# Kernel optimization log

Hardware: AMD Instinct MI355X
Metric: run time of the kernel (lower is better)

The kernel has to match this reference:

```python
import jax, jax.numpy as jnp
import numpy as np
from jax import lax

GRID_W, GRID_H = 4, 4
N_NODES = GRID_W * GRID_H  # 16
N_NEIGH = 8
N_CLS = 10
BN_EPS = 1e-5


def _neighbors(i, w, h, mode=8):
    # exact port of Brain.neighbors (ordering matters for the concat)
    size = w * h
    out = []
    if i - w >= 0:
        out.append(i - w)
    if i % w != 0:
        out.append(i - 1)
    if (i + 1) % w != 0:
        out.append(i + 1)
    if i + w < size:
        out.append(i + w)
    if mode == 8:
        if i - w - 1 >= 0 and i % w != 0:
            out.append(i - w - 1)
        if i - w + 1 >= 0 and (i + 1) % w != 0:
            out.append(i - w + 1)
        if i + w - 1 < size and i % w != 0:
            out.append(i + w - 1)
        if i + w + 1 < size and (i + 1) % w != 0:
            out.append(i + w + 1)
    return out


def _neighbor_table():
    idx = np.full((N_NODES, N_NEIGH), 0, dtype=np.int32)
    mask = np.zeros((N_NODES, N_NEIGH), dtype=np.float32)
    for i in range(N_NODES):
        n = _neighbors(i, GRID_W, GRID_H, 8)
        idx[i, :len(n)] = np.array(n, dtype=np.int32)
        mask[i, :len(n)] = 1.0
    return jnp.asarray(idx), jnp.asarray(mask)


def _conv(x, w, b):
    y = lax.conv_general_dilated(x, w, (1, 1), 'SAME',
                                 dimension_numbers=('NCHW', 'OIHW', 'NCHW'))
    return y + b[None, :, None, None]


def _bn_train(x, g, b):
    # BatchNorm2d in training mode (module default): batch statistics
    mean = jnp.mean(x, axis=(0, 2, 3), keepdims=True)
    var = jnp.var(x, axis=(0, 2, 3), keepdims=True)
    xn = (x - mean) * lax.rsqrt(var + BN_EPS)
    return xn * g[None, :, None, None] + b[None, :, None, None]


def _maxpool(x):
    # MaxPool2d(kernel=3, stride=2, padding=1)
    return lax.reduce_window(x, -jnp.inf, lax.max,
                             (1, 1, 3, 3), (1, 1, 2, 2),
                             ((0, 0), (0, 0), (1, 1), (1, 1)))


def setup_inputs() -> dict:
    key = jax.random.key(0)
    ks = jax.random.split(key, 24)
    B = 128
    f32 = jnp.float32

    def rn(k, shape, scale):
        return jax.random.normal(k, shape, dtype=f32) * scale

    inp = {
        'x': rn(ks[0], (B, 3, 64, 64), 1.0),
        'cw1': rn(ks[1], (64, 3, 3, 3), 0.1), 'cb1': jnp.zeros((64,), f32),
        'bn1_g': jnp.ones((64,), f32), 'bn1_b': jnp.zeros((64,), f32),
        'cw2': rn(ks[2], (128, 64, 3, 3), 0.05), 'cb2': jnp.zeros((128,), f32),
        'bn2_g': jnp.ones((128,), f32), 'bn2_b': jnp.zeros((128,), f32),
        'cw3': rn(ks[3], (256, 128, 3, 3), 0.03), 'cb3': jnp.zeros((256,), f32),
        'cw4': rn(ks[4], (256, 256, 3, 3), 0.02), 'cb4': jnp.zeros((256,), f32),
        'cw5': rn(ks[5], (512, 256, 3, 3), 0.02), 'cb5': jnp.zeros((512,), f32),
        'cw6': rn(ks[6], (512, 512, 3, 3), 0.015), 'cb6': jnp.zeros((512,), f32),
        'cw7': rn(ks[7], (512, 512, 3, 3), 0.015), 'cb7': jnp.zeros((512,), f32),
        'W1': rn(ks[8], (N_NODES, 592, 600), 0.04), 'b1': jnp.zeros((N_NODES, 600), f32),
        'W2': rn(ks[9], (N_NODES, 600, N_CLS), 0.04), 'b2': jnp.zeros((N_NODES, N_CLS), f32),
    }
    return inp


def _backbone(x, cw1, cb1, bn1_g, bn1_b, cw2, cb2, bn2_g, bn2_b,
              cw3, cb3, cw4, cb4, cw5, cb5, cw6, cb6, cw7, cb7):
    h = _maxpool(jax.nn.relu(_bn_train(_conv(x, cw1, cb1), bn1_g, bn1_b)))
    h = _maxpool(jax.nn.relu(_bn_train(_conv(h, cw2, cb2), bn2_g, bn2_b)))
    h = jax.nn.relu(_conv(h, cw3, cb3))
    h = _maxpool(jax.nn.relu(_conv(h, cw4, cb4)))
    h = jax.nn.relu(_conv(h, cw5, cb5))
    h = _maxpool(jax.nn.relu(_conv(h, cw6, cb6)))
    h = jax.nn.relu(_conv(h, cw7, cb7))
    return h  # [B, 512, 4, 4]


def _colons(X, W1, b1, W2, b2):
    # X: [16, B, 592] -> softmax probs [16, B, 10]; per-node MLP
    h = jnp.tanh(jnp.einsum('nbi,nio->nbo', X, W1) + b1[:, None, :])
    logits = jnp.einsum('nbh,nho->nbo', h, W2) + b2[:, None, :]
    return jax.nn.softmax(logits, axis=-1)


def reference(x, cw1, cb1, bn1_g, bn1_b, cw2, cb2, bn2_g, bn2_b,
              cw3, cb3, cw4, cb4, cw5, cb5, cw6, cb6, cw7, cb7,
              W1, b1, W2, b2):
    B = x.shape[0]
    conv = _backbone(x, cw1, cb1, bn1_g, bn1_b, cw2, cb2, bn2_g, bn2_b,
                     cw3, cb3, cw4, cb4, cw5, cb5, cw6, cb6, cw7, cb7)
    conv = conv.reshape(B, 512, N_NODES)           # torch.flatten(conv, 2)
    feats = jnp.transpose(conv, (2, 0, 1))         # [16, B, 512]

    # first pass: neighbor slots are all-zero p1..p8
    zeros80 = jnp.zeros((N_NODES, B, N_NEIGH * N_CLS), dtype=x.dtype)
    preds1 = _colons(jnp.concatenate([zeros80, feats], axis=-1), W1, b1, W2, b2)

    # second pass: gather neighbor predictions (zero-padded to 8 slots)
    idx, mask = _neighbor_table()                  # [16,8] int, [16,8] float
    gathered = preds1[idx]                         # [16, 8, B, 10]
    gathered = gathered * mask[:, :, None, None]
    neigh = jnp.transpose(gathered, (0, 2, 1, 3)).reshape(N_NODES, B, N_NEIGH * N_CLS)
    preds2 = _colons(jnp.concatenate([neigh, feats], axis=-1), W1, b1, W2, b2)  # [16, B, 10]

    sum_preds = jnp.mean(preds2, axis=0)           # [B, 10]
    squared_sum_preds = sum_preds * sum_preds
    return squared_sum_preds, preds2
```

## Files before the change

### kernel.cpp

```cpp
#include <hip/hip_runtime.h>
#include <math.h>


#define BN_EPS 1e-5f

typedef _Float16 f16x8 __attribute__((ext_vector_type(8)));
typedef _Float16 f16x4 __attribute__((ext_vector_type(4)));
typedef float    f32x4v __attribute__((ext_vector_type(4)));

constexpr int ilog2c(int x) { return x <= 1 ? 0 : 1 + ilog2c(x >> 1); }

__global__ __launch_bounds__(256)
void wsplit_kernel(const float* __restrict__ w, _Float16* __restrict__ o, int COCI)
{
    const int t = blockIdx.x * 256 + threadIdx.x;
    if (t >= COCI) return;
#pragma unroll
    for (int ph = 0; ph < 9; ++ph)
        o[ph * COCI + t] = (_Float16)w[t * 9 + ph];
}

__global__ void wsplit1_kernel(const float* __restrict__ w, _Float16* __restrict__ o)
{
    const int co = threadIdx.x;
#pragma unroll
    for (int k = 0; k < 32; ++k)
        o[co * 32 + k] = (k < 27) ? (_Float16)w[co * 27 + k] : (_Float16)0.f;
}

__global__ __launch_bounds__(256)
void w1t_kernel(const float* __restrict__ W1, _Float16* __restrict__ Tf,
                _Float16* __restrict__ Tn)
{
    __shared__ float T[64][65];
    const int n  = blockIdx.z;
    const int o0 = blockIdx.y * 64;
    const int k0 = blockIdx.x * 64;
    const int tid = threadIdx.x;
    const int c  = tid & 63;
    const int r4 = tid >> 6;
    const float* Wn = W1 + (size_t)n * 592 * 600;
#pragma unroll
    for (int rep = 0; rep < 16; ++rep) {
        const int kr = rep * 4 + r4;
        const int k = k0 + kr, o = o0 + c;
        float v = 0.f;
        if (k < 592 && o < 600) v = Wn[k * 600 + o];
        T[kr][c] = v;
    }
    __syncthreads();
#pragma unroll
    for (int rep = 0; rep < 16; ++rep) {
        const int orr = rep * 4 + r4;
        const int o = o0 + orr;
        const int k = k0 + c;
        const float v = T[c][orr];
        if (k >= 80 && k < 592)
            Tf[((size_t)(n * 640 + o)) * 512 + (k - 80)] = (_Float16)v;
        if (k < 96)
            Tn[((size_t)(n * 640 + o)) * 96 + k] = (k < 80) ? (_Float16)v : (_Float16)0.f;
    }
}

__global__ void b1pad_kernel(const float* __restrict__ b1, float* __restrict__ b1p)
{
    const int t = blockIdx.x * 256 + threadIdx.x;
    if (t >= 16 * 640) return;
    const int n = t / 640, o = t - n * 640;
    b1p[t] = (o < 600) ? b1[n * 600 + o] : 0.f;
}

__global__ __launch_bounds__(256)
void conv1_mfma_kernel(const float* __restrict__ in, const _Float16* __restrict__ w32,
                       _Float16* __restrict__ out, int B)
{
    __shared__ __align__(16) _Float16 As[64 * 32];
    __shared__ __align__(16) _Float16 Bs[128 * 32];

    const int tid  = threadIdx.x;
    const int pix0 = blockIdx.x * 128;
    const int bn   = tid & 127;
    const int bh   = tid >> 7;
    const int gp   = pix0 + bn;
    const int pb   = gp >> 12;
    const int sp   = gp & 4095;
    const int py   = sp >> 6;
    const int px   = sp & 63;
    const float* inb = in + (size_t)pb * 3 * 4096;

    _Float16 vals[16];
    if (bh == 0) {
#pragma unroll
        for (int u = 0; u < 16; ++u) {
            const int k = u;
            const int ci = k / 9, r = k - ci * 9, ky = r / 3, kx = r - ky * 3;
            const int iy = py + ky - 1, ix = px + kx - 1;
            float v = 0.f;
            if ((unsigned)iy < 64u && (unsigned)ix < 64u)
                v = inb[ci * 4096 + iy * 64 + ix];
            vals[u] = (_Float16)v;
        }
    } else {
#pragma unroll
        for (int u = 0; u < 16; ++u) {
            const int k = 16 + u;
            float v = 0.f;
            if (k < 27) {
                const int ci = k / 9, r = k - ci * 9, ky = r / 3, kx = r - ky * 3;
                const int iy = py + ky - 1, ix = px + kx - 1;
                if ((unsigned)iy < 64u && (unsigned)ix < 64u)
                    v = inb[ci * 4096 + iy * 64 + ix];
            }
            vals[u] = (_Float16)v;
        }
    }
    f16x8 b0, b1;
#pragma unroll
    for (int j = 0; j < 8; ++j) { b0[j] = vals[j]; b1[j] = vals[8 + j]; }
    *(f16x8*)&Bs[bn * 32 + (((2 * bh    ) ^ (bn & 3)) << 3)] = b0;
    *(f16x8*)&Bs[bn * 32 + (((2 * bh + 1) ^ (bn & 3)) << 3)] = b1;

    if (tid < 128) {
        const int arow = tid >> 1, ah = tid & 1;
        const f16x8 a0 = *(const f16x8*)(w32 + arow * 32 + ah * 16);
        const f16x8 a1 = *(const f16x8*)(w32 + arow * 32 + ah * 16 + 8);
        *(f16x8*)&As[arow * 32 + (((2 * ah    ) ^ (arow & 3)) << 3)] = a0;
        *(f16x8*)&As[arow * 32 + (((2 * ah + 1) ^ (arow & 3)) << 3)] = a1;
    }
    __syncthreads();

    const int lane = tid & 63, wv = tid >> 6;
    const int q = lane >> 4, lm = lane & 15;
    const int swz = (q ^ (lm & 3)) << 3;

    f16x8 af[4], bf[2];
#pragma unroll
    for (int ti = 0; ti < 4; ++ti)
        af[ti] = *(const f16x8*)&As[(ti * 16 + lm) * 32 + swz];
#pragma unroll
    for (int tj = 0; tj < 2; ++tj)
        bf[tj] = *(const f16x8*)&Bs[(wv * 32 + tj * 16 + lm) * 32 + swz];

    f32x4v acc[4][2];
#pragma unroll
    for (int ti = 0; ti < 4; ++ti)
#pragma unroll
        for (int tj = 0; tj < 2; ++tj)
            acc[ti][tj] = __builtin_amdgcn_mfma_f32_16x16x32_f16(
                af[ti], bf[tj], (f32x4v)0.f, 0, 0, 0);

#pragma unroll
    for (int tj = 0; tj < 2; ++tj) {
        const int gpix = pix0 + wv * 32 + tj * 16 + lm;
#pragma unroll
        for (int ti = 0; ti < 4; ++ti) {
            const int cob = ti * 16 + q * 4;
            f16x4 h4;
#pragma unroll
            for (int r = 0; r < 4; ++r) h4[r] = (_Float16)acc[ti][tj][r];
            *(f16x4*)&out[(size_t)gpix * 64 + cob] = h4;
        }
    }
}

template <int CI, int CO, int H, int W, int KSPLIT, int EPI>
__global__ __launch_bounds__(256)
void conv_bd_kernel(const _Float16* __restrict__ in, const _Float16* __restrict__ w9,
                    const float* __restrict__ bias, _Float16* __restrict__ out,
                    float* __restrict__ part, int B)
{
    constexpr int HW   = H * W;
    constexpr int lgHW = ilog2c(HW);
    constexpr int lgW  = ilog2c(W);

    __shared__ __align__(16) _Float16 As[2][128 * 32];

    const int tid  = threadIdx.x;
    const int pix0 = blockIdx.x * 128;
    const int co0  = blockIdx.y * 128;

    const int lane = tid & 63, wv = tid >> 6;
    const int wm = (wv & 1) * 64, wn = (wv >> 1) * 64;
    const int q = lane >> 4, lm = lane & 15;
    const int swz = (q ^ (lm & 3)) << 3;

    const int arow = tid >> 1, ah = tid & 1;
    const int aw0 = ((2 * ah    ) ^ (arow & 3)) << 3;
    const int aw1 = ((2 * ah + 1) ^ (arow & 3)) << 3;
    const _Float16* abase = w9 + ((size_t)(co0 + arow)) * CI + ah * 16;

    int pbq[4], pyq[4], pxq[4];
#pragma unroll
    for (int tj = 0; tj < 4; ++tj) {
        const int gp = pix0 + wn + tj * 16 + lm;
        pbq[tj] = gp >> lgHW;
        const int sp = gp & (HW - 1);
        pyq[tj] = sp >> lgW;
        pxq[tj] = sp & (W - 1);
    }

    f32x4v acc[4][4];
#pragma unroll
    for (int i = 0; i < 4; ++i)
#pragma unroll
        for (int j = 0; j < 4; ++j) acc[i][j] = (f32x4v)0.f;

    constexpr int CS_TOT = CI / 32;
    constexpr int CS_PER = CS_TOT / KSPLIT;
    const int cs0 = (KSPLIT > 1) ? blockIdx.z * CS_PER : 0;

    int buf = 0;
    for (int ph = 0; ph < 9; ++ph) {
        const int dy = ph / 3 - 1;
        const int dx = ph - (ph / 3) * 3 - 1;
        const _Float16* bb[4];
        f16x8 mskv[4];
#pragma unroll
        for (int tj = 0; tj < 4; ++tj) {
            const int y2 = pyq[tj] + dy, x2 = pxq[tj] + dx;
            const bool valid = ((unsigned)y2 < (unsigned)H) && ((unsigned)x2 < (unsigned)W);
            const int sp2 = valid ? ((y2 << lgW) | x2) : 0;
            bb[tj] = in + ((size_t)((pbq[tj] << lgHW) | sp2)) * CI + q * 8 + cs0 * 32;
            const _Float16 m = valid ? (_Float16)1.f : (_Float16)0.f;
#pragma unroll
            for (int j = 0; j < 8; ++j) mskv[tj][j] = m;
        }
        const _Float16* aph = abase + (size_t)ph * CO * CI + cs0 * 32;

        {
            const f16x8 a0 = *(const f16x8*)(aph);
            const f16x8 a1 = *(const f16x8*)(aph + 8);
            __syncthreads();
            *(f16x8*)&As[buf][arow * 32 + aw0] = a0;
            *(f16x8*)&As[buf][arow * 32 + aw1] = a1;
        }
        for (int cs = 0; cs < CS_PER; ++cs) {
            f16x8 bfr[4];
#pragma unroll
            for (int tj = 0; tj < 4; ++tj)
                bfr[tj] = *(const f16x8*)(bb[tj] + cs * 32);
            f16x8 aN0, aN1;
            if (cs + 1 < CS_PER) {
                aN0 = *(const f16x8*)(aph + (cs + 1) * 32);
                aN1 = *(const f16x8*)(aph + (cs + 1) * 32 + 8);
            }
            __syncthreads();
            f16x8 afr[4];
#pragma unroll
            for (int ti = 0; ti < 4; ++ti)
                afr[ti] = *(const f16x8*)&As[buf][(wm + ti * 16 + lm) * 32 + swz];
#pragma unroll
            for (int tj = 0; tj < 4; ++tj) bfr[tj] *= mskv[tj];
#pragma unroll
            for (int ti = 0; ti < 4; ++ti)
#pragma unroll
                for (int tj = 0; tj < 4; ++tj)
                    acc[ti][tj] = __builtin_amdgcn_mfma_f32_16x16x32_f16(
                        afr[ti], bfr[tj], acc[ti][tj], 0, 0, 0);
            if (cs + 1 < CS_PER) {
                *(f16x8*)&As[buf ^ 1][arow * 32 + aw0] = aN0;
                *(f16x8*)&As[buf ^ 1][arow * 32 + aw1] = aN1;
                buf ^= 1;
            }
        }
    }

    if (EPI == 2) {
        float* pout = part + (size_t)blockIdx.z * ((size_t)B * HW * CO);
#pragma unroll
        for (int tj = 0; tj < 4; ++tj) {
            const int gpix = pix0 + wn + tj * 16 + lm;
#pragma unroll
            for (int ti = 0; ti < 4; ++ti) {
                const int cob = co0 + wm + ti * 16 + q * 4;
                *(float4*)&pout[(size_t)gpix * CO + cob] =
                    make_float4(acc[ti][tj][0], acc[ti][tj][1],
                                acc[ti][tj][2], acc[ti][tj][3]);
            }
        }
    } else {
#pragma unroll
        for (int tj = 0; tj < 4; ++tj) {
            const int gpix = pix0 + wn + tj * 16 + lm;
#pragma unroll
            for (int ti = 0; ti < 4; ++ti) {
                const int cob = co0 + wm + ti * 16 + q * 4;
                f16x4 h4;
                if (EPI == 1) {
                    const float4 bb4 = *(const float4*)&bias[cob];
                    h4[0] = (_Float16)fmaxf(acc[ti][tj][0] + bb4.x, 0.f);
                    h4[1] = (_Float16)fmaxf(acc[ti][tj][1] + bb4.y, 0.f);
                    h4[2] = (_Float16)fmaxf(acc[ti][tj][2] + bb4.z, 0.f);
                    h4[3] = (_Float16)fmaxf(acc[ti][tj][3] + bb4.w, 0.f);
                } else {
#pragma unroll
                    for (int r = 0; r < 4; ++r) h4[r] = (_Float16)acc[ti][tj][r];
                }
                *(f16x4*)&out[(size_t)gpix * CO + cob] = h4;
            }
        }
    }
}

template <int C>
__global__ __launch_bounds__(256)
void bn_stats_nhwc_kernel(const _Float16* __restrict__ in, float* __restrict__ sums,
                          int Ptot)
{
    constexpr int C8 = C / 8;
    constexpr int PS = 256 / C8;
    const int chunk = Ptot / gridDim.x;
    const int c8   = threadIdx.x & (C8 - 1);
    const int poff = threadIdx.x >> ilog2c(C8);
    float s[8], s2[8];
#pragma unroll
    for (int j = 0; j < 8; ++j) { s[j] = 0.f; s2[j] = 0.f; }
    const int p0 = blockIdx.x * chunk;
    for (int p = p0 + poff; p < p0 + chunk; p += PS) {
        const f16x8 v = *(const f16x8*)(in + (size_t)p * C + c8 * 8);
#pragma unroll
        for (int j = 0; j < 8; ++j) {
            const float f = (float)v[j];
            s[j] += f; s2[j] += f * f;
        }
    }
    __shared__ float ls[2 * C];
    for (int i = threadIdx.x; i < 2 * C; i += 256) ls[i] = 0.f;
    __syncthreads();
#pragma unroll
    for (int j = 0; j < 8; ++j) {
        atomicAdd(&ls[c8 * 8 + j], s[j]);
        atomicAdd(&ls[C + c8 * 8 + j], s2[j]);
    }
    __syncthreads();
    for (int i = threadIdx.x; i < 2 * C; i += 256) atomicAdd(&sums[i], ls[i]);
}

template <int C>
__global__ void bn_finalize_kernel(const float* __restrict__ sums,
                                   const float* __restrict__ g,
                                   const float* __restrict__ beta,
                                   float* __restrict__ ss, int Ntot)
{
    const int c = blockIdx.x * 64 + threadIdx.x;
    if (c >= C) return;
    const float inv   = 1.f / (float)Ntot;
    const float mean  = sums[c] * inv;
    const float var   = sums[C + c] * inv - mean * mean;
    const float scale = g[c] * rsqrtf(var + BN_EPS);
    ss[c]     = scale;
    ss[C + c] = beta[c] - mean * scale;
}

template <int C, int Hin, int Win, bool DO_BN>
__global__ __launch_bounds__(256)
void pool_nhwc_kernel(const _Float16* __restrict__ in, const float* __restrict__ ss,
                      _Float16* __restrict__ out, int B)
{
    constexpr int Ho = Hin / 2, Wo = Win / 2, C8 = C / 8;
    constexpr int lgC8 = ilog2c(C8), lgWo = ilog2c(Wo), lgHo = ilog2c(Ho);
    const int t = blockIdx.x * 256 + threadIdx.x;
    const int total = B * Ho * Wo * C8;
    if (t >= total) return;
    const int c8 = t & (C8 - 1);
    const int r1 = t >> lgC8;
    const int ox = r1 & (Wo - 1);
    const int r2 = r1 >> lgWo;
    const int oy = r2 & (Ho - 1);
    const int b  = r2 >> lgHo;

    float sc[8], sh[8];
    if (DO_BN) {
#pragma unroll
        for (int j = 0; j < 8; ++j) {
            sc[j] = ss[c8 * 8 + j];
            sh[j] = ss[C + c8 * 8 + j];
        }
    }
    float m[8];
#pragma unroll
    for (int j = 0; j < 8; ++j) m[j] = -1e30f;

    const int y0 = max(0, 2 * oy - 1), y1 = min(Hin - 1, 2 * oy + 1);
    const int x0 = max(0, 2 * ox - 1), x1 = min(Win - 1, 2 * ox + 1);
    const _Float16* ib = in + ((size_t)b * Hin * Win) * C + c8 * 8;
    for (int iy = y0; iy <= y1; ++iy)
        for (int ix = x0; ix <= x1; ++ix) {
            const f16x8 v = *(const f16x8*)(ib + (size_t)(iy * Win + ix) * C);
#pragma unroll
            for (int j = 0; j < 8; ++j) {
                float f = (float)v[j];
                if (DO_BN) f = f * sc[j] + sh[j];
                m[j] = fmaxf(m[j], f);
            }
        }
    f16x8 o;
#pragma unroll
    for (int j = 0; j < 8; ++j) {
        float f = m[j];
        if (DO_BN) f = fmaxf(f, 0.f);
        o[j] = (_Float16)f;
    }
    *(f16x8*)&out[((size_t)((b << (lgHo + lgWo)) | (oy << lgWo) | ox)) * C + c8 * 8] = o;
}

template <int CO, int Z>
__global__ __launch_bounds__(256)
void sum_bias_relu_nhwc_kernel(const float* __restrict__ part, const float* __restrict__ bias,
                               _Float16* __restrict__ out, int Npix)
{
    const int t = blockIdx.x * 256 + threadIdx.x;
    const int N8 = Npix * CO / 8;
    if (t >= N8) return;
    const size_t i8 = (size_t)t * 8;
    const int c = (int)(i8 & (CO - 1));
    const size_t S = (size_t)Npix * CO;
    float4 x0 = *(const float4*)(part + i8);
    float4 x1 = *(const float4*)(part + i8 + 4);
#pragma unroll
    for (int z = 1; z < Z; ++z) {
        const float4 p0 = *(const float4*)(part + z * S + i8);
        const float4 p1 = *(const float4*)(part + z * S + i8 + 4);
        x0.x += p0.x; x0.y += p0.y; x0.z += p0.z; x0.w += p0.w;
        x1.x += p1.x; x1.y += p1.y; x1.z += p1.z; x1.w += p1.w;
    }
    const float4 b0 = *(const float4*)(bias + c);
    const float4 b1 = *(const float4*)(bias + c + 4);
    f16x8 o;
    o[0] = (_Float16)fmaxf(x0.x + b0.x, 0.f);
    o[1] = (_Float16)fmaxf(x0.y + b0.y, 0.f);
    o[2] = (_Float16)fmaxf(x0.z + b0.z, 0.f);
    o[3] = (_Float16)fmaxf(x0.w + b0.w, 0.f);
    o[4] = (_Float16)fmaxf(x1.x + b1.x, 0.f);
    o[5] = (_Float16)fmaxf(x1.y + b1.y, 0.f);
    o[6] = (_Float16)fmaxf(x1.z + b1.z, 0.f);
    o[7] = (_Float16)fmaxf(x1.w + b1.w, 0.f);
    *(f16x8*)&out[i8] = o;
}

template <int Z>
__global__ __launch_bounds__(256)
void build_xf_kernel(const float* __restrict__ part, const float* __restrict__ bias,
                     _Float16* __restrict__ Xf, int B)
{
    const int t = blockIdx.x * 256 + threadIdx.x;
    if (t >= B * 16 * 128) return;
    const int pix = t >> 7;
    const int c   = (t & 127) * 4;
    const size_t S = (size_t)B * 16 * 512;
    float4 a = *(const float4*)(part + (size_t)pix * 512 + c);
#pragma unroll
    for (int z = 1; z < Z; ++z) {
        const float4 p = *(const float4*)(part + z * S + (size_t)pix * 512 + c);
        a.x += p.x; a.y += p.y; a.z += p.z; a.w += p.w;
    }
    const float4 bb = *(const float4*)(bias + c);
    f16x4 o4;
    o4[0] = (_Float16)fmaxf(a.x + bb.x, 0.f);
    o4[1] = (_Float16)fmaxf(a.y + bb.y, 0.f);
    o4[2] = (_Float16)fmaxf(a.z + bb.z, 0.f);
    o4[3] = (_Float16)fmaxf(a.w + bb.w, 0.f);
    const int b_ = pix >> 4, sp = pix & 15;
    *(f16x4*)&Xf[((size_t)(sp * B + b_)) * 512 + c] = o4;
}

template <int K, bool PASS2>
__global__ __launch_bounds__(256)
void fc1_mfma_kernel(const _Float16* __restrict__ Xf, const _Float16* __restrict__ W1T,
                     const float* __restrict__ b1p, float* __restrict__ pre,
                     float* __restrict__ h, int B)
{
    __shared__ __align__(16) _Float16 As[2][128 * 32];
    __shared__ __align__(16) _Float16 Bs[2][128 * 32];

    const int tid = threadIdx.x;
    const int o0  = blockIdx.x * 128;
    const int n   = blockIdx.y;

    const int lane = tid & 63, wv = tid >> 6;
    const int wm = (wv & 1) * 64, wn = (wv >> 1) * 64;
    const int q = lane >> 4, lm = lane & 15;
    const int swz = (q ^ (lm & 3)) << 3;

    const int arow = tid >> 1, ah = tid & 1;
    const int aw0 = ((2 * ah    ) ^ (arow & 3)) << 3;
    const int aw1 = ((2 * ah + 1) ^ (arow & 3)) << 3;

    const _Float16* asrc = W1T + ((size_t)(n * 640 + o0 + arow)) * K + ah * 16;
    const _Float16* bsrc = Xf  + ((size_t)(n * 128 + arow)) * K + ah * 16;

    f32x4v acc[4][4];
#pragma unroll
    for (int i = 0; i < 4; ++i)
#pragma unroll
        for (int j = 0; j < 4; ++j) acc[i][j] = (f32x4v)0.f;

    constexpr int S = K / 32;
    {
        const f16x8 a0 = *(const f16x8*)(asrc);
        const f16x8 a1 = *(const f16x8*)(asrc + 8);
        const f16x8 b0 = *(const f16x8*)(bsrc);
        const f16x8 b1 = *(const f16x8*)(bsrc + 8);
        *(f16x8*)&As[0][arow * 32 + aw0] = a0;
        *(f16x8*)&As[0][arow * 32 + aw1] = a1;
        *(f16x8*)&Bs[0][arow * 32 + aw0] = b0;
        *(f16x8*)&Bs[0][arow * 32 + aw1] = b1;
    }
    int buf = 0;
    for (int s = 0; s < S; ++s) {
        f16x8 aN0, aN1, bN0, bN1;
        if (s + 1 < S) {
            aN0 = *(const f16x8*)(asrc + (s + 1) * 32);
            aN1 = *(const f16x8*)(asrc + (s + 1) * 32 + 8);
            bN0 = *(const f16x8*)(bsrc + (s + 1) * 32);
            bN1 = *(const f16x8*)(bsrc + (s + 1) * 32 + 8);
        }
        __syncthreads();
        f16x8 afr[4], bfr[4];
#pragma unroll
        for (int ti = 0; ti < 4; ++ti)
            afr[ti] = *(const f16x8*)&As[buf][(wm + ti * 16 + lm) * 32 + swz];
#pragma unroll
        for (int tj = 0; tj < 4; ++tj)
            bfr[tj] = *(const f16x8*)&Bs[buf][(wn + tj * 16 + lm) * 32 + swz];
#pragma unroll
        for (int ti = 0; ti < 4; ++ti)
#pragma unroll
            for (int tj = 0; tj < 4; ++tj)
                acc[ti][tj] = __builtin_amdgcn_mfma_f32_16x16x32_f16(
                    afr[ti], bfr[tj], acc[ti][tj], 0, 0, 0);
        if (s + 1 < S) {
            *(f16x8*)&As[buf ^ 1][arow * 32 + aw0] = aN0;
            *(f16x8*)&As[buf ^ 1][arow * 32 + aw1] = aN1;
            *(f16x8*)&Bs[buf ^ 1][arow * 32 + aw0] = bN0;
            *(f16x8*)&Bs[buf ^ 1][arow * 32 + aw1] = bN1;
            buf ^= 1;
        }
    }

#pragma unroll
    for (int tj = 0; tj < 4; ++tj) {
        const int m = wn + tj * 16 + lm;
#pragma unroll
        for (int ti = 0; ti < 4; ++ti) {
            const int o = o0 + wm + ti * 16 + q * 4;
            const size_t oi = ((size_t)(n * 128 + m)) * 640 + o;
            float4 base;
            if (PASS2) base = *(const float4*)&pre[oi];
            else       base = *(const float4*)&b1p[n * 640 + o];
            float4 v = make_float4(acc[ti][tj][0] + base.x, acc[ti][tj][1] + base.y,
                                   acc[ti][tj][2] + base.z, acc[ti][tj][3] + base.w);
            if (!PASS2) *(float4*)&pre[oi] = v;
            *(float4*)&h[oi] = make_float4(tanhf(v.x), tanhf(v.y), tanhf(v.z), tanhf(v.w));
        }
    }
}

__global__ __launch_bounds__(128)
void colon_fc2_kernel(const float* __restrict__ h, const float* __restrict__ W2,
                      const float* __restrict__ b2, float* __restrict__ preds, int B)
{
    const int n = blockIdx.x;
    __shared__ float W2s[6000];
    __shared__ float b2s[10];
    for (int i = threadIdx.x; i < 6000; i += 128) W2s[i] = W2[n * 6000 + i];
    if (threadIdx.x < 10) b2s[threadIdx.x] = b2[n * 10 + threadIdx.x];
    __syncthreads();

    for (int b = threadIdx.x; b < B; b += 128) {
        float l[10];
#pragma unroll
        for (int c = 0; c < 10; ++c) l[c] = b2s[c];
        const float* hp = h + ((size_t)(n * B + b)) * 640;
        for (int k = 0; k < 600; k += 4) {
            const float4 hv = *reinterpret_cast<const float4*>(&hp[k]);
            const float hh[4] = {hv.x, hv.y, hv.z, hv.w};
#pragma unroll
            for (int u = 0; u < 4; ++u)
#pragma unroll
                for (int c = 0; c < 10; ++c)
                    l[c] += hh[u] * W2s[(k + u) * 10 + c];
        }
        float mx = l[0];
#pragma unroll
        for (int c = 1; c < 10; ++c) mx = fmaxf(mx, l[c]);
        float s = 0.f;
#pragma unroll
        for (int c = 0; c < 10; ++c) { l[c] = expf(l[c] - mx); s += l[c]; }
        const float inv = 1.f / s;
        float* pp = preds + ((size_t)(n * B + b)) * 10;
#pragma unroll
        for (int c = 0; c < 10; ++c) pp[c] = l[c] * inv;
    }
}

__global__ __launch_bounds__(256)
void fill_neigh_kernel(const float* __restrict__ preds1, _Float16* __restrict__ Xn, int B)
{
    const int t = blockIdx.x * 256 + threadIdx.x;
    if (t >= 16 * B * 96) return;
    const int col = t % 96;
    const int b   = (t / 96) % B;
    const int n   = t / (96 * B);

    float v = 0.f;
    if (col < 80) {
        const int j = col / 10, c = col - j * 10;
        int lst[8];
        int cnt = 0;
        const int w = 4, sz = 16, i = n;
        if (i - w >= 0)                                lst[cnt++] = i - w;
        if (i % w != 0)                                lst[cnt++] = i - 1;
        if ((i + 1) % w != 0)                          lst[cnt++] = i + 1;
        if (i + w < sz)                                lst[cnt++] = i + w;
        if (i - w - 1 >= 0 && i % w != 0)              lst[cnt++] = i - w - 1;
        if (i - w + 1 >= 0 && (i + 1) % w != 0)        lst[cnt++] = i - w + 1;
        if (i + w - 1 < sz && i % w != 0)              lst[cnt++] = i + w - 1;
        if (i + w + 1 < sz && (i + 1) % w != 0)        lst[cnt++] = i + w + 1;
        if (j < cnt) v = preds1[((size_t)(lst[j] * B + b)) * 10 + c];
    }
    Xn[t] = (_Float16)v;
}

__global__ __launch_bounds__(256)
void final_out_kernel(const float* __restrict__ preds2, float* __restrict__ out0, int B)
{
    const int t = blockIdx.x * 256 + threadIdx.x;
    if (t >= B * 10) return;
    const int b = t / 10, c = t % 10;
    float s = 0.f;
#pragma unroll
    for (int n = 0; n < 16; ++n)
        s += preds2[((size_t)(n * B + b)) * 10 + c];
    const float m = s * (1.f / 16.f);
    out0[t] = m * m;
}

extern "C" void kernel_launch(void* const* d_in, const int* in_sizes, int n_in,
                              void* d_out, int out_size, void* d_ws, size_t ws_size,
                              hipStream_t stream)
{
    const float* x    = (const float*)d_in[0];
    const float* cw1  = (const float*)d_in[1];
    const float* bn1g = (const float*)d_in[3];
    const float* bn1b = (const float*)d_in[4];
    const float* cw2  = (const float*)d_in[5];
    const float* bn2g = (const float*)d_in[7];
    const float* bn2b = (const float*)d_in[8];
    const float* cw3  = (const float*)d_in[9];
    const float* cb3  = (const float*)d_in[10];
    const float* cw4  = (const float*)d_in[11];
    const float* cb4  = (const float*)d_in[12];
    const float* cw5  = (const float*)d_in[13];
    const float* cb5  = (const float*)d_in[14];
    const float* cw6  = (const float*)d_in[15];
    const float* cb6  = (const float*)d_in[16];
    const float* cw7  = (const float*)d_in[17];
    const float* cb7  = (const float*)d_in[18];
    const float* W1   = (const float*)d_in[19];
    const float* b1   = (const float*)d_in[20];
    const float* W2   = (const float*)d_in[21];
    const float* b2   = (const float*)d_in[22];

    const int B = in_sizes[0] / (3 * 64 * 64);

    float* ws = (float*)d_ws;
    float*     P    = ws;
    _Float16*  A    = (_Float16*)(ws + 8388608);
    _Float16*  Bb   = (_Float16*)(ws + 25165824);
    _Float16*  wreg = (_Float16*)(ws + 33554432);
    _Float16*  W1Tf = (_Float16*)(ws + 36984832);
    _Float16*  W1Tn = (_Float16*)(ws + 39606272);
    _Float16*  Xf16 = (_Float16*)(ws + 40097792);
    _Float16*  Xn16 = (_Float16*)(ws + 40622080);
    float*     b1p  = ws + 40720384;
    float*     preb = ws + 40730624;
    float*     hb   = ws + 42041344;
    float*     small= ws + 43352064;
    float* sums1  = small;
    float* sums2  = small + 256;
    float* ss1    = small + 1024;
    float* ss2    = small + 1536;
    float* preds1 = small + 2048;

    _Float16* w1f  = wreg;
    _Float16* w9c2 = wreg + 2048;
    _Float16* w9c3 = w9c2 + 73728;
    _Float16* w9c4 = w9c3 + 294912;
    _Float16* w9c5 = w9c4 + 589824;
    _Float16* w9c6 = w9c5 + 1179648;
    _Float16* w9c7 = w9c6 + 2359296;

    float* out0   = (float*)d_out;
    float* preds2 = (float*)d_out + (size_t)B * 10;

    hipMemsetAsync(small, 0, 512 * sizeof(float), stream);

    wsplit1_kernel<<<1, 64, 0, stream>>>(cw1, w1f);
    wsplit_kernel<<<(128 * 64  + 255) / 256, 256, 0, stream>>>(cw2, w9c2, 128 * 64);
    wsplit_kernel<<<(256 * 128 + 255) / 256, 256, 0, stream>>>(cw3, w9c3, 256 * 128);
    wsplit_kernel<<<(256 * 256 + 255) / 256, 256, 0, stream>>>(cw4, w9c4, 256 * 256);
    wsplit_kernel<<<(512 * 256 + 255) / 256, 256, 0, stream>>>(cw5, w9c5, 512 * 256);
    wsplit_kernel<<<(512 * 512 + 255) / 256, 256, 0, stream>>>(cw6, w9c6, 512 * 512);
    wsplit_kernel<<<(512 * 512 + 255) / 256, 256, 0, stream>>>(cw7, w9c7, 512 * 512);
    w1t_kernel<<<dim3(10, 10, 16), 256, 0, stream>>>(W1, W1Tf, W1Tn);
    b1pad_kernel<<<(16 * 640 + 255) / 256, 256, 0, stream>>>(b1, b1p);

    conv1_mfma_kernel<<<B * 4096 / 128, 256, 0, stream>>>(x, w1f, A, B);
    bn_stats_nhwc_kernel<64><<<512, 256, 0, stream>>>(A, sums1, B * 4096);
    bn_finalize_kernel<64><<<1, 64, 0, stream>>>(sums1, bn1g, bn1b, ss1, B * 4096);
    pool_nhwc_kernel<64, 64, 64, true>
        <<<(B * 1024 * 8 + 255) / 256, 256, 0, stream>>>(A, ss1, Bb, B);

    conv_bd_kernel<64, 128, 32, 32, 1, 0>
        <<<dim3(B * 1024 / 128, 1), 256, 0, stream>>>(Bb, w9c2, nullptr, A, nullptr, B);
    bn_stats_nhwc_kernel<128><<<256, 256, 0, stream>>>(A, sums2, B * 1024);
    bn_finalize_kernel<128><<<2, 64, 0, stream>>>(sums2, bn2g, bn2b, ss2, B * 1024);
    pool_nhwc_kernel<128, 32, 32, true>
        <<<(B * 256 * 16 + 255) / 256, 256, 0, stream>>>(A, ss2, Bb, B);

    conv_bd_kernel<128, 256, 16, 16, 1, 1>
        <<<dim3(B * 256 / 128, 2), 256, 0, stream>>>(Bb, w9c3, cb3, A, nullptr, B);
    conv_bd_kernel<256, 256, 16, 16, 1, 1>
        <<<dim3(B * 256 / 128, 2), 256, 0, stream>>>(A, w9c4, cb4, Bb, nullptr, B);
    pool_nhwc_kernel<256, 16, 16, false>
        <<<(B * 64 * 32 + 255) / 256, 256, 0, stream>>>(Bb, nullptr, A, B);

    conv_bd_kernel<256, 512, 8, 8, 2, 2>
        <<<dim3(B * 64 / 128, 4, 2), 256, 0, stream>>>(A, w9c5, nullptr, nullptr, P, B);
    sum_bias_relu_nhwc_kernel<512, 2>
        <<<(B * 64 * 512 / 8 + 255) / 256, 256, 0, stream>>>(P, cb5, Bb, B * 64);

    conv_bd_kernel<512, 512, 8, 8, 2, 2>
        <<<dim3(B * 64 / 128, 4, 2), 256, 0, stream>>>(Bb, w9c6, nullptr, nullptr, P, B);
    sum_bias_relu_nhwc_kernel<512, 2>
        <<<(B * 64 * 512 / 8 + 255) / 256, 256, 0, stream>>>(P, cb6, A, B * 64);
    pool_nhwc_kernel<512, 8, 8, false>
        <<<(B * 16 * 64 + 255) / 256, 256, 0, stream>>>(A, nullptr, Bb, B);

    conv_bd_kernel<512, 512, 4, 4, 8, 2>
        <<<dim3(B * 16 / 128, 4, 8), 256, 0, stream>>>(Bb, w9c7, nullptr, nullptr, P, B);

    build_xf_kernel<8><<<(B * 16 * 128 + 255) / 256, 256, 0, stream>>>(P, cb7, Xf16, B);

    fc1_mfma_kernel<512, false>
        <<<dim3(5, 16), 256, 0, stream>>>(Xf16, W1Tf, b1p, preb, hb, B);
    colon_fc2_kernel<<<16, 128, 0, stream>>>(hb, W2, b2, preds1, B);

    fill_neigh_kernel<<<(16 * B * 96 + 255) / 256, 256, 0, stream>>>(preds1, Xn16, B);
    fc1_mfma_kernel<96, true>
        <<<dim3(5, 16), 256, 0, stream>>>(Xn16, W1Tn, b1p, preb, hb, B);
    colon_fc2_kernel<<<16, 128, 0, stream>>>(hb, W2, b2, preds2, B);

    final_out_kernel<<<(B * 10 + 255) / 256, 256, 0, stream>>>(preds2, out0, B);
}
```

Before: 740.3 us.

## Flatten conv tap/channel loops into one software-pipelined loop with zero-buffer padding

Merges the 3x3 tap loop and channel-slice loop of the implicit-GEMM conv kernel into a single flat loop. B fragments are prefetched one iteration ahead in registers and A is double-buffered in LDS across tap boundaries, which removes the extra per-tap barrier. Out-of-bounds padding now points loads at a zeroed global buffer instead of multiplying by a mask. __syncthreads is replaced by a custom waitcnt lgkmcnt(0)+s_barrier so outstanding global prefetches are not drained at each barrier. The cost is higher register pressure from the bnext/bcur arrays and an extra memset.

```diff
diff --git a/kernel.cpp b/kernel.cpp
--- a/kernel.cpp
+++ b/kernel.cpp
@@ -9,6 +9,10 @@
 typedef float    f32x4v __attribute__((ext_vector_type(4)));
 
 constexpr int ilog2c(int x) { return x <= 1 ? 0 : 1 + ilog2c(x >> 1); }
+
+__device__ __forceinline__ void lds_barrier() {
+    asm volatile("s_waitcnt lgkmcnt(0)\n\ts_barrier" ::: "memory");
+}
 
 __global__ __launch_bounds__(256)
 void wsplit_kernel(const float* __restrict__ w, _Float16* __restrict__ o, int COCI)
@@ -165,9 +169,9 @@
 
 template <int CI, int CO, int H, int W, int KSPLIT, int EPI>
 __global__ __launch_bounds__(256)
-void conv_bd_kernel(const _Float16* __restrict__ in, const _Float16* __restrict__ w9,
+void conv_pl_kernel(const _Float16* __restrict__ in, const _Float16* __restrict__ w9,
                     const float* __restrict__ bias, _Float16* __restrict__ out,
-                    float* __restrict__ part, int B)
+                    float* __restrict__ part, const _Float16* __restrict__ zbuf, int B)
 {
     constexpr int HW   = H * W;
     constexpr int lgHW = ilog2c(HW);
@@ -199,69 +203,80 @@
         pxq[tj] = sp & (W - 1);
     }
 
-    f32x4v acc[4][4];
-#pragma unroll
-    for (int i = 0; i < 4; ++i)
-#pragma unroll
-        for (int j = 0; j < 4; ++j) acc[i][j] = (f32x4v)0.f;
-
     constexpr int CS_TOT = CI / 32;
     constexpr int CS_PER = CS_TOT / KSPLIT;
+    constexpr int NIT    = 9 * CS_PER;
     const int cs0 = (KSPLIT > 1) ? blockIdx.z * CS_PER : 0;
 
-    int buf = 0;
-    for (int ph = 0; ph < 9; ++ph) {
-        const int dy = ph / 3 - 1;
-        const int dx = ph - (ph / 3) * 3 - 1;
-        const _Float16* bb[4];
-        f16x8 mskv[4];
+    const _Float16* bp[4];
+    auto setB = [&](int phx) {
+        const int dy = phx / 3 - 1;
+        const int dx = phx - (phx / 3) * 3 - 1;
 #pragma unroll
         for (int tj = 0; tj < 4; ++tj) {
             const int y2 = pyq[tj] + dy, x2 = pxq[tj] + dx;
             const bool valid = ((unsigned)y2 < (unsigned)H) && ((unsigned)x2 < (unsigned)W);
-            const int sp2 = valid ? ((y2 << lgW) | x2) : 0;
-            bb[tj] = in + ((size_t)((pbq[tj] << lgHW) | sp2)) * CI + q * 8 + cs0 * 32;
-            const _Float16 m = valid ? (_Float16)1.f : (_Float16)0.f;
-#pragma unroll
-            for (int j = 0; j < 8; ++j) mskv[tj][j] = m;
-        }
-        const _Float16* aph = abase + (size_t)ph * CO * CI + cs0 * 32;
-
-        {
-            const f16x8 a0 = *(const f16x8*)(aph);
-            const f16x8 a1 = *(const f16x8*)(aph + 8);
-            __syncthreads();
-            *(f16x8*)&As[buf][arow * 32 + aw0] = a0;
-            *(f16x8*)&As[buf][arow * 32 + aw1] = a1;
-        }
-        for (int cs = 0; cs < CS_PER; ++cs) {
-            f16x8 bfr[4];
+            const int sp2 = (y2 << lgW) | x2;
+            bp[tj] = valid ? (in + ((size_t)((pbq[tj] << lgHW) | sp2)) * CI + q * 8)
+                           : (zbuf + q * 8);
+        }
+    };
+
+    f32x4v acc[4][4];
+#pragma unroll
+    for (int i = 0; i < 4; ++i)
+#pragma unroll
+        for (int j = 0; j < 4; ++j) acc[i][j] = (f32x4v)0.f;
+
+    setB(0);
+    f16x8 bcur[4];
+#pragma unroll
+    for (int tj = 0; tj < 4; ++tj)
+        bcur[tj] = *(const f16x8*)(bp[tj] + (size_t)cs0 * 32);
+    {
+        const f16x8 a0 = *(const f16x8*)(abase + (size_t)cs0 * 32);
+        const f16x8 a1 = *(const f16x8*)(abase + (size_t)cs0 * 32 + 8);
+        *(f16x8*)&As[0][arow * 32 + aw0] = a0;
+        *(f16x8*)&As[0][arow * 32 + aw1] = a1;
+    }
+
+    int buf = 0, ph = 0, cs = 0;
+    for (int it = 0; it < NIT; ++it) {
+        int phn = ph, csn = cs + 1;
+        const bool adv = (csn == CS_PER);
+        if (adv) { csn = 0; phn = ph + 1; }
+        const bool havenext = (it + 1 < NIT);
+        f16x8 bnext[4], aN0, aN1;
+        if (havenext) {
+            if (adv) setB(phn);
 #pragma unroll
             for (int tj = 0; tj < 4; ++tj)
-                bfr[tj] = *(const f16x8*)(bb[tj] + cs * 32);
-            f16x8 aN0, aN1;
-            if (cs + 1 < CS_PER) {
-                aN0 = *(const f16x8*)(aph + (cs + 1) * 32);
-                aN1 = *(const f16x8*)(aph + (cs + 1) * 32 + 8);
-            }
-            __syncthreads();
-            f16x8 afr[4];
-#pragma unroll
-            for (int ti = 0; ti < 4; ++ti)
-                afr[ti] = *(const f16x8*)&As[buf][(wm + ti * 16 + lm) * 32 + swz];
-#pragma unroll
-            for (int tj = 0; tj < 4; ++tj) bfr[tj] *= mskv[tj];
-#pragma unroll
-            for (int ti = 0; ti < 4; ++ti)
-#pragma unroll
-                for (int tj = 0; tj < 4; ++tj)
-                    acc[ti][tj] = __builtin_amdgcn_mfma_f32_16x16x32_f16(
-                        afr[ti], bfr[tj], acc[ti][tj], 0, 0, 0);
-            if (cs + 1 < CS_PER) {
-                *(f16x8*)&As[buf ^ 1][arow * 32 + aw0] = aN0;
-                *(f16x8*)&As[buf ^ 1][arow * 32 + aw1] = aN1;
-                buf ^= 1;
-            }
+                bnext[tj] = *(const f16x8*)(bp[tj] + (size_t)(cs0 + csn) * 32);
+            const _Float16* aphn = abase + (size_t)phn * CO * CI;
+            aN0 = *(const f16x8*)(aphn + (size_t)(cs0 + csn) * 32);
+            aN1 = *(const f16x8*)(aphn + (size_t)(cs0 + csn) * 32 + 8);
+        }
+
+        lds_barrier();
+
+        f16x8 afr[4];
+#pragma unroll
+        for (int ti = 0; ti < 4; ++ti)
+            afr[ti] = *(const f16x8*)&As[buf][(wm + ti * 16 + lm) * 32 + swz];
+#pragma unroll
+        for (int ti = 0; ti < 4; ++ti)
+#pragma unroll
+            for (int tj = 0; tj < 4; ++tj)
+                acc[ti][tj] = __builtin_amdgcn_mfma_f32_16x16x32_f16(
+                    afr[ti], bcur[tj], acc[ti][tj], 0, 0, 0);
+
+        if (havenext) {
+            *(f16x8*)&As[buf ^ 1][arow * 32 + aw0] = aN0;
+            *(f16x8*)&As[buf ^ 1][arow * 32 + aw1] = aN1;
+            buf ^= 1;
+#pragma unroll
+            for (int tj = 0; tj < 4; ++tj) bcur[tj] = bnext[tj];
+            ph = phn; cs = csn;
         }
     }
 
@@ -515,7 +530,7 @@
             bN0 = *(const f16x8*)(bsrc + (s + 1) * 32);
             bN1 = *(const f16x8*)(bsrc + (s + 1) * 32 + 8);
         }
-        __syncthreads();
+        lds_barrier();
         f16x8 afr[4], bfr[4];
 #pragma unroll
         for (int ti = 0; ti < 4; ++ti)
@@ -682,6 +697,7 @@
     float* ss1    = small + 1024;
     float* ss2    = small + 1536;
     float* preds1 = small + 2048;
+    _Float16* zbuf = (_Float16*)(small + 32768);
 
     _Float16* w1f  = wreg;
     _Float16* w9c2 = wreg + 2048;
@@ -695,6 +711,7 @@
     float* preds2 = (float*)d_out + (size_t)B * 10;
 
     hipMemsetAsync(small, 0, 512 * sizeof(float), stream);
+    hipMemsetAsync(zbuf, 0, 4096, stream);
 
     wsplit1_kernel<<<1, 64, 0, stream>>>(cw1, w1f);
     wsplit_kernel<<<(128 * 64  + 255) / 256, 256, 0, stream>>>(cw2, w9c2, 128 * 64);
@@ -712,34 +729,34 @@
     pool_nhwc_kernel<64, 64, 64, true>
         <<<(B * 1024 * 8 + 255) / 256, 256, 0, stream>>>(A, ss1, Bb, B);
 
-    conv_bd_kernel<64, 128, 32, 32, 1, 0>
-        <<<dim3(B * 1024 / 128, 1), 256, 0, stream>>>(Bb, w9c2, nullptr, A, nullptr, B);
+    conv_pl_kernel<64, 128, 32, 32, 1, 0>
+        <<<dim3(B * 1024 / 128, 1), 256, 0, stream>>>(Bb, w9c2, nullptr, A, nullptr, zbuf, B);
     bn_stats_nhwc_kernel<128><<<256, 256, 0, stream>>>(A, sums2, B * 1024);
     bn_finalize_kernel<128><<<2, 64, 0, stream>>>(sums2, bn2g, bn2b, ss2, B * 1024);
     pool_nhwc_kernel<128, 32, 32, true>
         <<<(B * 256 * 16 + 255) / 256, 256, 0, stream>>>(A, ss2, Bb, B);
 
-    conv_bd_kernel<128, 256, 16, 16, 1, 1>
-        <<<dim3(B * 256 / 128, 2), 256, 0, stream>>>(Bb, w9c3, cb3, A, nullptr, B);
-    conv_bd_kernel<256, 256, 16, 16, 1, 1>
-        <<<dim3(B * 256 / 128, 2), 256, 0, stream>>>(A, w9c4, cb4, Bb, nullptr, B);
+    conv_pl_kernel<128, 256, 16, 16, 1, 1>
+        <<<dim3(B * 256 / 128, 2), 256, 0, stream>>>(Bb, w9c3, cb3, A, nullptr, zbuf, B);
+    conv_pl_kernel<256, 256, 16, 16, 1, 1>
+        <<<dim3(B * 256 / 128, 2), 256, 0, stream>>>(A, w9c4, cb4, Bb, nullptr, zbuf, B);
     pool_nhwc_kernel<256, 16, 16, false>
         <<<(B * 64 * 32 + 255) / 256, 256, 0, stream>>>(Bb, nullptr, A, B);
 
-    conv_bd_kernel<256, 512, 8, 8, 2, 2>
-        <<<dim3(B * 64 / 128, 4, 2), 256, 0, stream>>>(A, w9c5, nullptr, nullptr, P, B);
+    conv_pl_kernel<256, 512, 8, 8, 2, 2>
+        <<<dim3(B * 64 / 128, 4, 2), 256, 0, stream>>>(A, w9c5, nullptr, nullptr, P, zbuf, B);
     sum_bias_relu_nhwc_kernel<512, 2>
         <<<(B * 64 * 512 / 8 + 255) / 256, 256, 0, stream>>>(P, cb5, Bb, B * 64);
 
-    conv_bd_kernel<512, 512, 8, 8, 2, 2>
-        <<<dim3(B * 64 / 128, 4, 2), 256, 0, stream>>>(Bb, w9c6, nullptr, nullptr, P, B);
+    conv_pl_kernel<512, 512, 8, 8, 2, 2>
+        <<<dim3(B * 64 / 128, 4, 2), 256, 0, stream>>>(Bb, w9c6, nullptr, nullptr, P, zbuf, B);
     sum_bias_relu_nhwc_kernel<512, 2>
         <<<(B * 64 * 512 / 8 + 255) / 256, 256, 0, stream>>>(P, cb6, A, B * 64);
     pool_nhwc_kernel<512, 8, 8, false>
         <<<(B * 16 * 64 + 255) / 256, 256, 0, stream>>>(A, nullptr, Bb, B);
 
-    conv_bd_kernel<512, 512, 4, 4, 8, 2>
-        <<<dim3(B * 16 / 128, 4, 8), 256, 0, stream>>>(Bb, w9c7, nullptr, nullptr, P, B);
+    conv_pl_kernel<512, 512, 4, 4, 8, 2>
+        <<<dim3(B * 16 / 128, 4, 8), 256, 0, stream>>>(Bb, w9c7, nullptr, nullptr, P, zbuf, B);
 
     build_xf_kernel<8><<<(B * 16 * 128 + 255) / 256, 256, 0, stream>>>(P, cb7, Xf16, B);
 
```

After: 732.9 us. About the same (-1.0%).
